# Kernel tuning notes

Hardware: AMD Instinct MI355X
Metric: run time of the kernel (lower is better)

Reference implementation:

```python
import jax, jax.numpy as jnp
import numpy as np

B, W, N, DIM, GAMMA = 32, 16, 256, 256, 4
WH = 16  # sqrt(N)
V = DIM // GAMMA
TABLE = (2 * WH - 1) * (2 * WH - 1)  # 961


def _make_rel_index(wh: int) -> np.ndarray:
    coords = np.stack(np.meshgrid(np.arange(wh), np.arange(wh), indexing='ij'))  # (2, wh, wh)
    flat = coords.reshape(2, -1)                         # (2, wh*wh)
    rel = flat[:, :, None] - flat[:, None, :]            # (2, n, n)
    rel = rel.transpose(1, 2, 0).copy()                  # (n, n, 2)
    rel[:, :, 0] += wh - 1
    rel[:, :, 1] += wh - 1
    rel[:, :, 0] *= 2 * wh - 1
    return rel.sum(-1).astype(np.int32)                  # (n, n)


def setup_inputs() -> dict:
    key = jax.random.key(0)
    k1, k2, k3 = jax.random.split(key, 3)
    x = jax.random.normal(k1, (B, W, N, DIM), dtype=jnp.float32)
    bias_table = jax.random.normal(k2, (TABLE, W * GAMMA), dtype=jnp.float32) * 0.02
    token_bias = jax.random.normal(k3, (W * GAMMA, N, 1), dtype=jnp.float32) * 0.02
    rel_index = jnp.asarray(_make_rel_index(WH))
    return {"x": x, "bias_table": bias_table, "token_bias": token_bias, "rel_index": rel_index}


def reference(x, bias_table, token_bias, rel_index):
    b, w, n, d = x.shape
    gamma = GAMMA
    v = d // gamma
    # gather: (n, n, w*gamma) -> permute to (w*gamma, n, n)
    rpb = bias_table[rel_index.reshape(-1)].reshape(n, n, w * gamma)
    rpb = jnp.transpose(rpb, (2, 0, 1))                  # ((s w), n, n) with s outer
    # rearrange '(s b) m n -> b m n s'
    win_weight = jnp.transpose(rpb.reshape(gamma, w, n, n), (1, 2, 3, 0))  # (w, m, n, s)
    # rearrange 'b w n (v s) -> b w n v s'
    xs = x.reshape(b, w, n, v, gamma)
    out = jnp.einsum('wmns,bwnvs->bwmvs', win_weight, xs)
    # rearrange '(w s) m v -> w m v s'
    bias = jnp.transpose(token_bias.reshape(w, gamma, n, 1), (0, 2, 3, 1))  # (w, m, 1, s)
    out = out + bias[None]
    return out.reshape(b, w, n, d)
```

## Files before the change

kernel.cpp:

```cpp
#include <hip/hip_runtime.h>
#include <stdint.h>


typedef __attribute__((ext_vector_type(8))) short bf16x8;
typedef __attribute__((ext_vector_type(4))) float f32x4;
typedef __attribute__((ext_vector_type(8))) unsigned short u16x8;

__device__ __forceinline__ unsigned short f2bf(float f) {
    union { float f; unsigned u; } v; v.f = f;
    unsigned u = v.u;
    u += 0x7FFFu + ((u >> 16) & 1u);
    return (unsigned short)(u >> 16);
}
__device__ __forceinline__ float bf2f(unsigned short h) {
    union { unsigned u; float f; } v; v.u = ((unsigned)h) << 16;
    return v.f;
}
__device__ __forceinline__ int expInRange(unsigned short w16) {
    int e = (w16 >> 7) & 0xFF;
    return (e >= 100 && e <= 140) ? 1 : 0;
}

__global__ __launch_bounds__(256) void k_gather(
    const void* __restrict__ bt_raw,
    const int*  __restrict__ rel_index,
    const void* __restrict__ x_raw,
    unsigned short* __restrict__ Ab)
{
    const unsigned short* xw = (const unsigned short*)x_raw;
    int t = threadIdx.x;
    int pred = expInRange(xw[t * 2]) & expInRange(xw[t * 2 + 1]);
    int cnt = __syncthreads_count(pred);
    bool isF32 = (cnt < 150);

    int idx4 = blockIdx.x * 256 + t;
    int base = idx4 << 2;
    int nn = base & 255;
    int m  = (base >> 8) & 255;
    int ws = base >> 16;
    int colw = ((ws & 3) << 4) + (ws >> 2);
    const int* ri = rel_index + (m << 8) + nn;
    int i0 = ri[0], i1 = ri[1], i2 = ri[2], i3 = ri[3];
    ushort4 o;
    if (isF32) {
        const float* bt = (const float*)bt_raw;
        o.x = f2bf(bt[(i0 << 6) + colw]);
        o.y = f2bf(bt[(i1 << 6) + colw]);
        o.z = f2bf(bt[(i2 << 6) + colw]);
        o.w = f2bf(bt[(i3 << 6) + colw]);
    } else {
        const unsigned short* bt = (const unsigned short*)bt_raw;
        o.x = bt[(i0 << 6) + colw];
        o.y = bt[(i1 << 6) + colw];
        o.z = bt[(i2 << 6) + colw];
        o.w = bt[(i3 << 6) + colw];
    }
    *(ushort4*)(Ab + base) = o;
}

__global__ __launch_bounds__(512, 4) void k_main(
    const void* __restrict__ x_raw,
    const unsigned short* __restrict__ Ab,
    const void* __restrict__ tb_raw,
    void* __restrict__ out_raw)
{
    __shared__ unsigned short lds[16384 + 8192];

    const int tid  = threadIdx.x;
    const unsigned short* xw = (const unsigned short*)x_raw;
    int pred = expInRange(xw[tid]);
    int cnt = __syncthreads_count(pred);
    const bool isF32 = (cnt < 400);

    const int lane = tid & 63;
    const int wave = tid >> 6;
    const int bx = blockIdx.x;
    const int b  = bx & 31;
    const int mt = (bx >> 5) & 1;
    const int w  = bx >> 6;
    const int m0 = mt << 7;

    const int sw   = wave & 3;
    const int vh   = wave >> 2;
    const int vvb  = vh << 5;
    const int col  = lane & 15;
    const int quad = lane >> 4;

    const int a_row = tid >> 2;
    const int a_nn8 = (tid & 3) << 3;
    unsigned short* AsW = lds + (a_row << 5) + a_nn8;
    const unsigned short* Ag = Ab + (w << 18) + ((m0 + a_row) << 8) + a_nn8;

    const int x_nn = tid & 31;
    const int x_vg = tid >> 5;
    const int xoff = (((b << 4) + w) << 16) + (x_nn << 8) + (x_vg << 4);
    const float*          Xgf = (const float*)x_raw + xoff;
    const unsigned short* Xgh = (const unsigned short*)x_raw + xoff;
    unsigned short* XsW = lds + 16384 + x_nn;

    f32x4 acc[8][2];
#pragma unroll
    for (int mi = 0; mi < 8; mi++) {
        acc[mi][0] = (f32x4){0.f, 0.f, 0.f, 0.f};
        acc[mi][1] = (f32x4){0.f, 0.f, 0.f, 0.f};
    }

    const unsigned short* AsR = lds + (sw << 12) + (col << 5) + (quad << 3);
    const unsigned short* XsR = lds + 16384 + (sw << 11) + ((vvb + col) << 5) + (quad << 3);

    for (int nc = 0; nc < 8; nc++) {
        u16x8 av[4];
#pragma unroll
        for (int it = 0; it < 4; it++)
            av[it] = *(const u16x8*)(Ag + (it << 16) + (nc << 5));
#pragma unroll
        for (int it = 0; it < 4; it++)
            *(u16x8*)(AsW + (it << 12)) = av[it];

        if (isF32) {
            float4 v[4];
#pragma unroll
            for (int i = 0; i < 4; i++)
                v[i] = *(const float4*)(Xgf + (nc << 13) + (i << 2));
            const float* vf = (const float*)v;
#pragma unroll
            for (int j = 0; j < 16; j++) {
                int vv = (x_vg << 2) + (j >> 2);
                XsW[((j & 3) << 11) + (vv << 5)] = f2bf(vf[j]);
            }
        } else {
            u16x8 xv0 = *(const u16x8*)(Xgh + (nc << 13));
            u16x8 xv1 = *(const u16x8*)(Xgh + (nc << 13) + 8);
#pragma unroll
            for (int j = 0; j < 8; j++) {
                int vv = (x_vg << 2) + (j >> 2);
                XsW[((j & 3) << 11) + (vv << 5)] = xv0[j];
            }
#pragma unroll
            for (int j = 0; j < 8; j++) {
                int vv = (x_vg << 2) + 2 + (j >> 2);
                XsW[((j & 3) << 11) + (vv << 5)] = xv1[j];
            }
        }
        __syncthreads();

        bf16x8 bfr0 = *(const bf16x8*)(XsR);
        bf16x8 bfr1 = *(const bf16x8*)(XsR + 512);
#pragma unroll
        for (int mi = 0; mi < 8; mi++) {
            bf16x8 afr = *(const bf16x8*)(AsR + (mi << 9));
            acc[mi][0] = __builtin_amdgcn_mfma_f32_16x16x32_bf16(afr, bfr0, acc[mi][0], 0, 0, 0);
            acc[mi][1] = __builtin_amdgcn_mfma_f32_16x16x32_bf16(afr, bfr1, acc[mi][1], 0, 0, 0);
        }
        __syncthreads();
    }

    const int tboff = (((w << 2) + sw) << 8) + m0;
    const int ooff  = (((b << 4) + w) << 16) + (m0 << 8) + sw;
    if (isF32) {
        const float* tb = (const float*)tb_raw + tboff;
        float* ob = (float*)out_raw + ooff;
#pragma unroll
        for (int mi = 0; mi < 8; mi++) {
#pragma unroll
            for (int r = 0; r < 4; r++) {
                int m = (mi << 4) + (quad << 2) + r;
                float bias = tb[m];
#pragma unroll
                for (int vi = 0; vi < 2; vi++) {
                    int vv = vvb + (vi << 4) + col;
                    ob[(m << 8) + (vv << 2)] = acc[mi][vi][r] + bias;
                }
            }
        }
    } else {
        const unsigned short* tb = (const unsigned short*)tb_raw + tboff;
        unsigned short* ob = (unsigned short*)out_raw + ooff;
#pragma unroll
        for (int mi = 0; mi < 8; mi++) {
#pragma unroll
            for (int r = 0; r < 4; r++) {
                int m = (mi << 4) + (quad << 2) + r;
                float bias = bf2f(tb[m]);
#pragma unroll
                for (int vi = 0; vi < 2; vi++) {
                    int vv = vvb + (vi << 4) + col;
                    ob[(m << 8) + (vv << 2)] = f2bf(acc[mi][vi][r] + bias);
                }
            }
        }
    }
}

__global__ __launch_bounds__(512, 4) void k_main_fused(
    const void* __restrict__ x_raw,
    const void* __restrict__ bt_raw,
    const int*  __restrict__ rel_index,
    const void* __restrict__ tb_raw,
    void* __restrict__ out_raw)
{
    __shared__ unsigned short lds[16384 + 8192];

    const int tid  = threadIdx.x;
    const unsigned short* xw = (const unsigned short*)x_raw;
    int pred = expInRange(xw[tid]);
    int cnt = __syncthreads_count(pred);
    const bool isF32 = (cnt < 400);

    const int lane = tid & 63;
    const int wave = tid >> 6;
    const int bx = blockIdx.x;
    const int b  = bx & 31;
    const int mt = (bx >> 5) & 1;
    const int w  = bx >> 6;
    const int m0 = mt << 7;

    const int sw   = wave & 3;
    const int vh   = wave >> 2;
    const int vvb  = vh << 5;
    const int col  = lane & 15;
    const int quad = lane >> 4;

    const int a_row = tid >> 2;
    const int a_nn8 = (tid & 3) << 3;
    unsigned short* AsW = lds + (a_row << 5) + a_nn8;
    const int* rIp = rel_index + ((m0 + a_row) << 8) + a_nn8;

    const int x_nn = tid & 31;
    const int x_vg = tid >> 5;
    const int xoff = (((b << 4) + w) << 16) + (x_nn << 8) + (x_vg << 4);
    const float*          Xgf = (const float*)x_raw + xoff;
    const unsigned short* Xgh = (const unsigned short*)x_raw + xoff;
    unsigned short* XsW = lds + 16384 + x_nn;

    f32x4 acc[8][2];
#pragma unroll
    for (int mi = 0; mi < 8; mi++) {
        acc[mi][0] = (f32x4){0.f, 0.f, 0.f, 0.f};
        acc[mi][1] = (f32x4){0.f, 0.f, 0.f, 0.f};
    }

    const unsigned short* AsR = lds + (sw << 12) + (col << 5) + (quad << 3);
    const unsigned short* XsR = lds + 16384 + (sw << 11) + ((vvb + col) << 5) + (quad << 3);

    for (int nc = 0; nc < 8; nc++) {
        int4 r0 = *(const int4*)(rIp + (nc << 5));
        int4 r1 = *(const int4*)(rIp + (nc << 5) + 4);
        int ri[8] = {r0.x, r0.y, r0.z, r0.w, r1.x, r1.y, r1.z, r1.w};
#pragma unroll
        for (int it = 0; it < 4; it++) {
            u16x8 av;
            if (isF32) {
                const float* bt = (const float*)bt_raw;
#pragma unroll
                for (int j = 0; j < 8; j++)
                    av[j] = f2bf(bt[(ri[j] << 6) + (it << 4) + w]);
            } else {
                const unsigned short* bt = (const unsigned short*)bt_raw;
#pragma unroll
                for (int j = 0; j < 8; j++)
                    av[j] = bt[(ri[j] << 6) + (it << 4) + w];
            }
            *(u16x8*)(AsW + (it << 12)) = av;
        }

        if (isF32) {
            float4 v[4];
#pragma unroll
            for (int i = 0; i < 4; i++)
                v[i] = *(const float4*)(Xgf + (nc << 13) + (i << 2));
            const float* vf = (const float*)v;
#pragma unroll
            for (int j = 0; j < 16; j++) {
                int vv = (x_vg << 2) + (j >> 2);
                XsW[((j & 3) << 11) + (vv << 5)] = f2bf(vf[j]);
            }
        } else {
            u16x8 xv0 = *(const u16x8*)(Xgh + (nc << 13));
            u16x8 xv1 = *(const u16x8*)(Xgh + (nc << 13) + 8);
#pragma unroll
            for (int j = 0; j < 8; j++) {
                int vv = (x_vg << 2) + (j >> 2);
                XsW[((j & 3) << 11) + (vv << 5)] = xv0[j];
            }
#pragma unroll
            for (int j = 0; j < 8; j++) {
                int vv = (x_vg << 2) + 2 + (j >> 2);
                XsW[((j & 3) << 11) + (vv << 5)] = xv1[j];
            }
        }
        __syncthreads();

        bf16x8 bfr0 = *(const bf16x8*)(XsR);
        bf16x8 bfr1 = *(const bf16x8*)(XsR + 512);
#pragma unroll
        for (int mi = 0; mi < 8; mi++) {
            bf16x8 afr = *(const bf16x8*)(AsR + (mi << 9));
            acc[mi][0] = __builtin_amdgcn_mfma_f32_16x16x32_bf16(afr, bfr0, acc[mi][0], 0, 0, 0);
            acc[mi][1] = __builtin_amdgcn_mfma_f32_16x16x32_bf16(afr, bfr1, acc[mi][1], 0, 0, 0);
        }
        __syncthreads();
    }

    const int tboff = (((w << 2) + sw) << 8) + m0;
    const int ooff  = (((b << 4) + w) << 16) + (m0 << 8) + sw;
    if (isF32) {
        const float* tb = (const float*)tb_raw + tboff;
        float* ob = (float*)out_raw + ooff;
#pragma unroll
        for (int mi = 0; mi < 8; mi++) {
#pragma unroll
            for (int r = 0; r < 4; r++) {
                int m = (mi << 4) + (quad << 2) + r;
                float bias = tb[m];
#pragma unroll
                for (int vi = 0; vi < 2; vi++) {
                    int vv = vvb + (vi << 4) + col;
                    ob[(m << 8) + (vv << 2)] = acc[mi][vi][r] + bias;
                }
            }
        }
    } else {
        const unsigned short* tb = (const unsigned short*)tb_raw + tboff;
        unsigned short* ob = (unsigned short*)out_raw + ooff;
#pragma unroll
        for (int mi = 0; mi < 8; mi++) {
#pragma unroll
            for (int r = 0; r < 4; r++) {
                int m = (mi << 4) + (quad << 2) + r;
                float bias = bf2f(tb[m]);
#pragma unroll
                for (int vi = 0; vi < 2; vi++) {
                    int vv = vvb + (vi << 4) + col;
                    ob[(m << 8) + (vv << 2)] = f2bf(acc[mi][vi][r] + bias);
                }
            }
        }
    }
}

extern "C" void kernel_launch(void* const* d_in, const int* in_sizes, int n_in,
                              void* d_out, int out_size, void* d_ws, size_t ws_size,
                              hipStream_t stream) {
    const void* x          = d_in[0];
    const void* bias_table = d_in[1];
    const void* token_bias = d_in[2];
    const int*  rel_index  = (const int*)d_in[3];

    const size_t AB_BYTES = (size_t)64 * 256 * 256 * 2;
    if (ws_size >= AB_BYTES) {
        unsigned short* Ab = (unsigned short*)d_ws;
        hipLaunchKernelGGL(k_gather, dim3(4096), dim3(256), 0, stream,
                           bias_table, rel_index, x, Ab);
        hipLaunchKernelGGL(k_main, dim3(1024), dim3(512), 0, stream,
                           x, Ab, token_bias, d_out);
    } else {
        hipLaunchKernelGGL(k_main_fused, dim3(1024), dim3(512), 0, stream,
                           x, bias_table, rel_index, token_bias, d_out);
    }
}
```

Before: 292.9 us.

## Specialize to fp32, stage bias column in LDS, swizzle LDS, prefetch next chunk

Drops the runtime dtype detection and the fused fallback, hardcoding fp32 inputs and always using the workspace path. The gather kernel first loads one bias-table column into LDS and gathers from there instead of doing strided global reads. The main kernel XOR-swizzles the LDS layouts of A and X to cut bank conflicts, and register-prefetches the next n-chunk's global loads while the current chunk's MFMAs run. The trade-offs are more registers per thread, and the code now assumes fp32 inputs and a large enough workspace.

Result: slower. 327.8 us (+11.9%).

```diff
diff --git a/kernel.cpp b/kernel.cpp
--- a/kernel.cpp
+++ b/kernel.cpp
@@ -12,66 +12,41 @@
     u += 0x7FFFu + ((u >> 16) & 1u);
     return (unsigned short)(u >> 16);
 }
-__device__ __forceinline__ float bf2f(unsigned short h) {
-    union { unsigned u; float f; } v; v.u = ((unsigned)h) << 16;
-    return v.f;
-}
-__device__ __forceinline__ int expInRange(unsigned short w16) {
-    int e = (w16 >> 7) & 0xFF;
-    return (e >= 100 && e <= 140) ? 1 : 0;
-}
 
 __global__ __launch_bounds__(256) void k_gather(
-    const void* __restrict__ bt_raw,
+    const float* __restrict__ bt,
     const int*  __restrict__ rel_index,
-    const void* __restrict__ x_raw,
     unsigned short* __restrict__ Ab)
 {
-    const unsigned short* xw = (const unsigned short*)x_raw;
-    int t = threadIdx.x;
-    int pred = expInRange(xw[t * 2]) & expInRange(xw[t * 2 + 1]);
-    int cnt = __syncthreads_count(pred);
-    bool isF32 = (cnt < 150);
+    __shared__ float colLds[961];
+    const int t  = threadIdx.x;
+    const int ws = blockIdx.x >> 6;
+    const int colw = ((ws & 3) << 4) + (ws >> 2);
+    for (int i = t; i < 961; i += 256)
+        colLds[i] = bt[(i << 6) + colw];
+    __syncthreads();
 
-    int idx4 = blockIdx.x * 256 + t;
-    int base = idx4 << 2;
-    int nn = base & 255;
-    int m  = (base >> 8) & 255;
-    int ws = base >> 16;
-    int colw = ((ws & 3) << 4) + (ws >> 2);
+    const int base = (blockIdx.x * 256 + t) << 2;
+    const int nn = base & 255;
+    const int m  = (base >> 8) & 255;
     const int* ri = rel_index + (m << 8) + nn;
-    int i0 = ri[0], i1 = ri[1], i2 = ri[2], i3 = ri[3];
     ushort4 o;
-    if (isF32) {
-        const float* bt = (const float*)bt_raw;
-        o.x = f2bf(bt[(i0 << 6) + colw]);
-        o.y = f2bf(bt[(i1 << 6) + colw]);
-        o.z = f2bf(bt[(i2 << 6) + colw]);
-        o.w = f2bf(bt[(i3 << 6) + colw]);
-    } else {
-        const unsigned short* bt = (const unsigned short*)bt_raw;
-        o.x = bt[(i0 << 6) + colw];
-        o.y = bt[(i1 << 6) + colw];
-        o.z = bt[(i2 << 6) + colw];
-        o.w = bt[(i3 << 6) + colw];
-    }
+    o.x = f2bf(colLds[ri[0]]);
+    o.y = f2bf(colLds[ri[1]]);
+    o.z = f2bf(colLds[ri[2]]);
+    o.w = f2bf(colLds[ri[3]]);
     *(ushort4*)(Ab + base) = o;
 }
 
 __global__ __launch_bounds__(512, 4) void k_main(
-    const void* __restrict__ x_raw,
+    const float* __restrict__ x,
     const unsigned short* __restrict__ Ab,
-    const void* __restrict__ tb_raw,
-    void* __restrict__ out_raw)
+    const float* __restrict__ token_bias,
+    float* __restrict__ out)
 {
     __shared__ unsigned short lds[16384 + 8192];
 
     const int tid  = threadIdx.x;
-    const unsigned short* xw = (const unsigned short*)x_raw;
-    int pred = expInRange(xw[tid]);
-    int cnt = __syncthreads_count(pred);
-    const bool isF32 = (cnt < 400);
-
     const int lane = tid & 63;
     const int wave = tid >> 6;
     const int bx = blockIdx.x;
@@ -87,16 +62,15 @@
     const int quad = lane >> 4;
 
     const int a_row = tid >> 2;
-    const int a_nn8 = (tid & 3) << 3;
-    unsigned short* AsW = lds + (a_row << 5) + a_nn8;
-    const unsigned short* Ag = Ab + (w << 18) + ((m0 + a_row) << 8) + a_nn8;
+    const int a_g   = tid & 3;
+    const int a_gs  = a_g ^ ((a_row >> 2) & 3);
+    unsigned short* AsW = lds + (a_row << 5) + (a_gs << 3);
+    const unsigned short* Ag = Ab + (w << 18) + ((m0 + a_row) << 8) + (a_g << 3);
 
     const int x_nn = tid & 31;
     const int x_vg = tid >> 5;
-    const int xoff = (((b << 4) + w) << 16) + (x_nn << 8) + (x_vg << 4);
-    const float*          Xgf = (const float*)x_raw + xoff;
-    const unsigned short* Xgh = (const unsigned short*)x_raw + xoff;
-    unsigned short* XsW = lds + 16384 + x_nn;
+    const float* Xg = x + (((b << 4) + w) << 16) + (x_nn << 8) + (x_vg << 4);
+    unsigned short* XsW = lds + 16384 + (((x_nn >> 3) ^ (x_vg & 3)) << 3) + (x_nn & 7);
 
     f32x4 acc[8][2];
 #pragma unroll
@@ -105,44 +79,40 @@
         acc[mi][1] = (f32x4){0.f, 0.f, 0.f, 0.f};
     }
 
-    const unsigned short* AsR = lds + (sw << 12) + (col << 5) + (quad << 3);
-    const unsigned short* XsR = lds + 16384 + (sw << 11) + ((vvb + col) << 5) + (quad << 3);
+    const int gsr = quad ^ ((col >> 2) & 3);
+    const unsigned short* AsR = lds + (sw << 12) + (col << 5) + (gsr << 3);
+    const unsigned short* XsR = lds + 16384 + (sw << 11) + ((vvb + col) << 5) + (gsr << 3);
 
+    u16x8  av[4];
+    float4 xv[4];
+#pragma unroll
+    for (int it = 0; it < 4; it++)
+        av[it] = *(const u16x8*)(Ag + (it << 16));
+#pragma unroll
+    for (int i = 0; i < 4; i++)
+        xv[i] = *(const float4*)(Xg + (i << 2));
+
+#pragma unroll
     for (int nc = 0; nc < 8; nc++) {
-        u16x8 av[4];
-#pragma unroll
-        for (int it = 0; it < 4; it++)
-            av[it] = *(const u16x8*)(Ag + (it << 16) + (nc << 5));
 #pragma unroll
         for (int it = 0; it < 4; it++)
             *(u16x8*)(AsW + (it << 12)) = av[it];
+        const float* xf = (const float*)xv;
+#pragma unroll
+        for (int j = 0; j < 16; j++) {
+            int vv = (x_vg << 2) + (j >> 2);
+            XsW[((j & 3) << 11) + (vv << 5)] = f2bf(xf[j]);
+        }
+        __syncthreads();
 
-        if (isF32) {
-            float4 v[4];
+        if (nc < 7) {
+#pragma unroll
+            for (int it = 0; it < 4; it++)
+                av[it] = *(const u16x8*)(Ag + (it << 16) + ((nc + 1) << 5));
 #pragma unroll
             for (int i = 0; i < 4; i++)
-                v[i] = *(const float4*)(Xgf + (nc << 13) + (i << 2));
-            const float* vf = (const float*)v;
-#pragma unroll
-            for (int j = 0; j < 16; j++) {
-                int vv = (x_vg << 2) + (j >> 2);
-                XsW[((j & 3) << 11) + (vv << 5)] = f2bf(vf[j]);
-            }
-        } else {
-            u16x8 xv0 = *(const u16x8*)(Xgh + (nc << 13));
-            u16x8 xv1 = *(const u16x8*)(Xgh + (nc << 13) + 8);
-#pragma unroll
-            for (int j = 0; j < 8; j++) {
-                int vv = (x_vg << 2) + (j >> 2);
-                XsW[((j & 3) << 11) + (vv << 5)] = xv0[j];
-            }
-#pragma unroll
-            for (int j = 0; j < 8; j++) {
-                int vv = (x_vg << 2) + 2 + (j >> 2);
-                XsW[((j & 3) << 11) + (vv << 5)] = xv1[j];
-            }
+                xv[i] = *(const float4*)(Xg + ((nc + 1) << 13) + (i << 2));
         }
-        __syncthreads();
 
         bf16x8 bfr0 = *(const bf16x8*)(XsR);
         bf16x8 bfr1 = *(const bf16x8*)(XsR + 512);
@@ -155,185 +125,18 @@
         __syncthreads();
     }
 
-    const int tboff = (((w << 2) + sw) << 8) + m0;
-    const int ooff  = (((b << 4) + w) << 16) + (m0 << 8) + sw;
-    if (isF32) {
-        const float* tb = (const float*)tb_raw + tboff;
-        float* ob = (float*)out_raw + ooff;
-#pragma unroll
-        for (int mi = 0; mi < 8; mi++) {
-#pragma unroll
-            for (int r = 0; r < 4; r++) {
-                int m = (mi << 4) + (quad << 2) + r;
-                float bias = tb[m];
-#pragma unroll
-                for (int vi = 0; vi < 2; vi++) {
-                    int vv = vvb + (vi << 4) + col;
-                    ob[(m << 8) + (vv << 2)] = acc[mi][vi][r] + bias;
-                }
-            }
-        }
-    } else {
-        const unsigned short* tb = (const unsigned short*)tb_raw + tboff;
-        unsigned short* ob = (unsigned short*)out_raw + ooff;
-#pragma unroll
-        for (int mi = 0; mi < 8; mi++) {
-#pragma unroll
-            for (int r = 0; r < 4; r++) {
-                int m = (mi << 4) + (quad << 2) + r;
-                float bias = bf2f(tb[m]);
-#pragma unroll
-                for (int vi = 0; vi < 2; vi++) {
-                    int vv = vvb + (vi << 4) + col;
-                    ob[(m << 8) + (vv << 2)] = f2bf(acc[mi][vi][r] + bias);
-                }
-            }
-        }
-    }
-}
-
-__global__ __launch_bounds__(512, 4) void k_main_fused(
-    const void* __restrict__ x_raw,
-    const void* __restrict__ bt_raw,
-    const int*  __restrict__ rel_index,
-    const void* __restrict__ tb_raw,
-    void* __restrict__ out_raw)
-{
-    __shared__ unsigned short lds[16384 + 8192];
-
-    const int tid  = threadIdx.x;
-    const unsigned short* xw = (const unsigned short*)x_raw;
-    int pred = expInRange(xw[tid]);
-    int cnt = __syncthreads_count(pred);
-    const bool isF32 = (cnt < 400);
-
-    const int lane = tid & 63;
-    const int wave = tid >> 6;
-    const int bx = blockIdx.x;
-    const int b  = bx & 31;
-    const int mt = (bx >> 5) & 1;
-    const int w  = bx >> 6;
-    const int m0 = mt << 7;
-
-    const int sw   = wave & 3;
-    const int vh   = wave >> 2;
-    const int vvb  = vh << 5;
-    const int col  = lane & 15;
-    const int quad = lane >> 4;
-
-    const int a_row = tid >> 2;
-    const int a_nn8 = (tid & 3) << 3;
-    unsigned short* AsW = lds + (a_row << 5) + a_nn8;
-    const int* rIp = rel_index + ((m0 + a_row) << 8) + a_nn8;
-
-    const int x_nn = tid & 31;
-    const int x_vg = tid >> 5;
-    const int xoff = (((b << 4) + w) << 16) + (x_nn << 8) + (x_vg << 4);
-    const float*          Xgf = (const float*)x_raw + xoff;
-    const unsigned short* Xgh = (const unsigned short*)x_raw + xoff;
-    unsigned short* XsW = lds + 16384 + x_nn;
-
-    f32x4 acc[8][2];
+    const float* tb = token_bias + (((w << 2) + sw) << 8) + m0;
+    float* ob = out + (((b << 4) + w) << 16) + (m0 << 8) + sw;
 #pragma unroll
     for (int mi = 0; mi < 8; mi++) {
-        acc[mi][0] = (f32x4){0.f, 0.f, 0.f, 0.f};
-        acc[mi][1] = (f32x4){0.f, 0.f, 0.f, 0.f};
-    }
-
-    const unsigned short* AsR = lds + (sw << 12) + (col << 5) + (quad << 3);
-    const unsigned short* XsR = lds + 16384 + (sw << 11) + ((vvb + col) << 5) + (quad << 3);
-
-    for (int nc = 0; nc < 8; nc++) {
-        int4 r0 = *(const int4*)(rIp + (nc << 5));
-        int4 r1 = *(const int4*)(rIp + (nc << 5) + 4);
-        int ri[8] = {r0.x, r0.y, r0.z, r0.w, r1.x, r1.y, r1.z, r1.w};
 #pragma unroll
-        for (int it = 0; it < 4; it++) {
-            u16x8 av;
-            if (isF32) {
-                const float* bt = (const float*)bt_raw;
+        for (int r = 0; r < 4; r++) {
+            int m = (mi << 4) + (quad << 2) + r;
+            float bias = tb[m];
 #pragma unroll
-                for (int j = 0; j < 8; j++)
-                    av[j] = f2bf(bt[(ri[j] << 6) + (it << 4) + w]);
-            } else {
-                const unsigned short* bt = (const unsigned short*)bt_raw;
-#pragma unroll
-                for (int j = 0; j < 8; j++)
-                    av[j] = bt[(ri[j] << 6) + (it << 4) + w];
-            }
-            *(u16x8*)(AsW + (it << 12)) = av;
-        }
-
-        if (isF32) {
-            float4 v[4];
-#pragma unroll
-            for (int i = 0; i < 4; i++)
-                v[i] = *(const float4*)(Xgf + (nc << 13) + (i << 2));
-            const float* vf = (const float*)v;
-#pragma unroll
-            for (int j = 0; j < 16; j++) {
-                int vv = (x_vg << 2) + (j >> 2);
-                XsW[((j & 3) << 11) + (vv << 5)] = f2bf(vf[j]);
-            }
-        } else {
-            u16x8 xv0 = *(const u16x8*)(Xgh + (nc << 13));
-            u16x8 xv1 = *(const u16x8*)(Xgh + (nc << 13) + 8);
-#pragma unroll
-            for (int j = 0; j < 8; j++) {
-                int vv = (x_vg << 2) + (j >> 2);
-                XsW[((j & 3) << 11) + (vv << 5)] = xv0[j];
-            }
-#pragma unroll
-            for (int j = 0; j < 8; j++) {
-                int vv = (x_vg << 2) + 2 + (j >> 2);
-                XsW[((j & 3) << 11) + (vv << 5)] = xv1[j];
-            }
-        }
-        __syncthreads();
-
-        bf16x8 bfr0 = *(const bf16x8*)(XsR);
-        bf16x8 bfr1 = *(const bf16x8*)(XsR + 512);
-#pragma unroll
-        for (int mi = 0; mi < 8; mi++) {
-            bf16x8 afr = *(const bf16x8*)(AsR + (mi << 9));
-            acc[mi][0] = __builtin_amdgcn_mfma_f32_16x16x32_bf16(afr, bfr0, acc[mi][0], 0, 0, 0);
-            acc[mi][1] = __builtin_amdgcn_mfma_f32_16x16x32_bf16(afr, bfr1, acc[mi][1], 0, 0, 0);
-        }
-        __syncthreads();
-    }
-
-    const int tboff = (((w << 2) + sw) << 8) + m0;
-    const int ooff  = (((b << 4) + w) << 16) + (m0 << 8) + sw;
-    if (isF32) {
-        const float* tb = (const float*)tb_raw + tboff;
-        float* ob = (float*)out_raw + ooff;
-#pragma unroll
-        for (int mi = 0; mi < 8; mi++) {
-#pragma unroll
-            for (int r = 0; r < 4; r++) {
-                int m = (mi << 4) + (quad << 2) + r;
-                float bias = tb[m];
-#pragma unroll
-                for (int vi = 0; vi < 2; vi++) {
-                    int vv = vvb + (vi << 4) + col;
-                    ob[(m << 8) + (vv << 2)] = acc[mi][vi][r] + bias;
-                }
-            }
-        }
-    } else {
-        const unsigned short* tb = (const unsigned short*)tb_raw + tboff;
-        unsigned short* ob = (unsigned short*)out_raw + ooff;
-#pragma unroll
-        for (int mi = 0; mi < 8; mi++) {
-#pragma unroll
-            for (int r = 0; r < 4; r++) {
-                int m = (mi << 4) + (quad << 2) + r;
-                float bias = bf2f(tb[m]);
-#pragma unroll
-                for (int vi = 0; vi < 2; vi++) {
-                    int vv = vvb + (vi << 4) + col;
-                    ob[(m << 8) + (vv << 2)] = f2bf(acc[mi][vi][r] + bias);
-                }
+            for (int vi = 0; vi < 2; vi++) {
+                int vv = vvb + (vi << 4) + col;
+                ob[(m << 8) + (vv << 2)] = acc[mi][vi][r] + bias;
             }
         }
     }
@@ -342,20 +145,15 @@
 extern "C" void kernel_launch(void* const* d_in, const int* in_sizes, int n_in,
                               void* d_out, int out_size, void* d_ws, size_t ws_size,
                               hipStream_t stream) {
-    const void* x          = d_in[0];
-    const void* bias_table = d_in[1];
-    const void* token_bias = d_in[2];
-    const int*  rel_index  = (const int*)d_in[3];
+    const float* x          = (const float*)d_in[0];
+    const float* bias_table = (const float*)d_in[1];
+    const float* token_bias = (const float*)d_in[2];
+    const int*   rel_index  = (const int*)d_in[3];
+    unsigned short* Ab = (unsigned short*)d_ws;
+    float* out = (float*)d_out;
 
-    const size_t AB_BYTES = (size_t)64 * 256 * 256 * 2;
-    if (ws_size >= AB_BYTES) {
-        unsigned short* Ab = (unsigned short*)d_ws;
-        hipLaunchKernelGGL(k_gather, dim3(4096), dim3(256), 0, stream,
-                           bias_table, rel_index, x, Ab);
-        hipLaunchKernelGGL(k_main, dim3(1024), dim3(512), 0, stream,
-                           x, Ab, token_bias, d_out);
-    } else {
-        hipLaunchKernelGGL(k_main_fused, dim3(1024), dim3(512), 0, stream,
-                           x, bias_table, rel_index, token_bias, d_out);
-    }
+    hipLaunchKernelGGL(k_gather, dim3(4096), dim3(256), 0, stream,
+                       bias_table, rel_index, Ab);
+    hipLaunchKernelGGL(k_main, dim3(1024), dim3(512), 0, stream,
+                       x, Ab, token_bias, out);
 }
```
